# Optimization experiments

Hardware: AMD Instinct MI355X
Metric: run time of the kernel (lower is better)

## Reference

```python
import jax, jax.numpy as jnp
import numpy as np

SEQ, BS, IN, HS = 512, 64, 1024, 1024


def _xavier(key, shape):
    fan_in, fan_out = shape
    limit = np.sqrt(6.0 / (fan_in + fan_out)).astype(np.float32)
    return jax.random.uniform(key, shape, jnp.float32, -limit, limit)


def setup_inputs() -> dict:
    key = jax.random.key(0)
    k1, k2, k3, k4, k5 = jax.random.split(key, 5)
    return {
        "x": jax.random.normal(k1, (SEQ, BS, IN), jnp.float32),
        "h0": jax.random.normal(k2, (1, BS, HS), jnp.float32),
        "c0": jax.random.normal(k3, (1, BS, HS), jnp.float32),
        "weight_ih": _xavier(k4, (IN, 4 * HS)),
        "weight_hh": _xavier(k5, (HS, 4 * HS)),
        "bias": jnp.zeros((4 * HS,), jnp.float32),
    }


def reference(x, h0, c0, weight_ih, weight_hh, bias):
    HSd = weight_hh.shape[0]
    # Precompute the input projection for all timesteps in one big GEMM.
    x_gates = jnp.einsum('sbi,ih->sbh', x, weight_ih) + bias  # [S, B, 4H]

    def step(carry, xg_t):
        h_t, c_t = carry
        gates = xg_t + h_t @ weight_hh  # [B, 4H]
        i_t = jax.nn.sigmoid(gates[:, :HSd])
        f_t = jax.nn.sigmoid(gates[:, HSd:2 * HSd])
        g_t = jnp.tanh(gates[:, 2 * HSd:3 * HSd])
        o_t = jax.nn.sigmoid(gates[:, 3 * HSd:])
        c_t = f_t * c_t + i_t * g_t
        h_t = o_t * jnp.tanh(c_t)
        return (h_t, c_t), h_t

    (h_T, c_T), hidden_seq = jax.lax.scan(step, (h0[0], c0[0]), x_gates)
    return hidden_seq, (h_T[None], c_T[None])
```

## Files before the change

### kernel.cpp

```cpp
#include <hip/hip_runtime.h>
#include <stdint.h>


typedef unsigned short u16;
typedef __attribute__((ext_vector_type(8))) short bf16x8;
typedef __attribute__((ext_vector_type(2))) uint64_t u64x2;
typedef __attribute__((ext_vector_type(4))) float f32x4;

static __device__ __forceinline__ u16 f2b(float f) {
  uint32_t b = __float_as_uint(f);
  return (u16)((b + 0x7fffu + ((b >> 16) & 1u)) >> 16);
}
static __device__ __forceinline__ uint64_t pack4(float4 v) {
  return (uint64_t)f2b(v.x) | ((uint64_t)f2b(v.y) << 16) |
         ((uint64_t)f2b(v.z) << 32) | ((uint64_t)f2b(v.w) << 48);
}
static __device__ __forceinline__ float b2f(u16 u) {
  return __uint_as_float(((uint32_t)u) << 16);
}
static __device__ __forceinline__ float sigm(float x) {
  return 1.0f / (1.0f + __expf(-x));
}
static __device__ __forceinline__ float tanh_(float x) {
  float e = __expf(2.0f * x);
  return 1.0f - 2.0f / (e + 1.0f);
}

__global__ __launch_bounds__(256) void transpose_w(const float* __restrict__ Wih,
                                                   const float* __restrict__ Whh,
                                                   u16* __restrict__ Tih,
                                                   u16* __restrict__ Thh) {
  __shared__ float tile[64][65];
  const float* src = blockIdx.z ? Whh : Wih;
  u16* dst = blockIdx.z ? Thh : Tih;
  int k0 = blockIdx.y * 64, n0 = blockIdx.x * 64;
  int tid = threadIdx.x;
#pragma unroll
  for (int i = 0; i < 16; ++i) {
    int idx = i * 256 + tid;
    int kl = idx >> 6, nl = idx & 63;
    tile[kl][nl] = src[(size_t)(k0 + kl) * 4096 + n0 + nl];
  }
  __syncthreads();
#pragma unroll
  for (int i = 0; i < 16; ++i) {
    int idx = i * 256 + tid;
    int nl = idx >> 6, kl = idx & 63;
    dst[(size_t)(n0 + nl) * 1024 + k0 + kl] = f2b(tile[kl][nl]);
  }
}

__global__ __launch_bounds__(256) void convert_h0(const float* __restrict__ h0,
                                                  uint64_t* __restrict__ dst) {
  int i = blockIdx.x * 256 + threadIdx.x;
  float2 v = ((const float2*)h0)[i];
  uint32_t pair = (uint32_t)f2b(v.x) | ((uint32_t)f2b(v.y) << 16);
  dst[i] = (uint64_t)pair;
}

__global__ __launch_bounds__(256) void gemm_xg(const float* __restrict__ A,
                                               const u16* __restrict__ Bt,
                                               const float* __restrict__ bias,
                                               u16* __restrict__ C) {
  __shared__ u16 sA[2][128 * 32];
  __shared__ u16 sB[2][128 * 32];
  const int tid = threadIdx.x;
  const int wave = tid >> 6, lane = tid & 63;
  const int bx = blockIdx.x, by = blockIdx.y;
  const int wr = wave >> 1, wc = wave & 1;
  const int lm = lane & 15, ko = (lane >> 4) * 8;

  const int ar = lane >> 1, ac = (lane & 1) * 16;
  const float* gA = A + (size_t)(by * 128 + wave * 32 + ar) * 1024 + ac;
  const u16* gB = Bt + (size_t)(bx * 128 + wave * 32 + (lane >> 2)) * 1024 + (lane & 3) * 8;
  const int bidx = wave * 1024 + (lane >> 2) * 32 + (lane & 3) * 8;

  f32x4 acc[4][4] = {};

  auto stage = [&](int kt, int buf) {
    const u16* gb = gB + kt * 32;
    bf16x8 b0 = *(const bf16x8*)gb;
    bf16x8 b1 = *(const bf16x8*)(gb + 16 * 1024);
    *(bf16x8*)&sB[buf][bidx] = b0;
    *(bf16x8*)&sB[buf][bidx + 512] = b1;
    const float* ga = gA + kt * 32;
    float4 v0 = *(const float4*)(ga + 0);
    float4 v1 = *(const float4*)(ga + 4);
    float4 v2 = *(const float4*)(ga + 8);
    float4 v3 = *(const float4*)(ga + 12);
    uint64_t* la = (uint64_t*)&sA[buf][wave * 1024 + ar * 32 + ac];
    la[0] = pack4(v0);
    la[1] = pack4(v1);
    la[2] = pack4(v2);
    la[3] = pack4(v3);
  };

  stage(0, 0);
  __syncthreads();
  int p = 0;
  for (int kt = 0; kt < 32; ++kt) {
    if (kt < 31) stage(kt + 1, p ^ 1);
    bf16x8 af[4], bfv[4];
#pragma unroll
    for (int i = 0; i < 4; ++i)
      af[i] = *(const bf16x8*)&sA[p][(wr * 64 + i * 16 + lm) * 32 + ko];
#pragma unroll
    for (int j = 0; j < 4; ++j)
      bfv[j] = *(const bf16x8*)&sB[p][(wc * 64 + j * 16 + lm) * 32 + ko];
#pragma unroll
    for (int i = 0; i < 4; ++i)
#pragma unroll
      for (int j = 0; j < 4; ++j)
        acc[i][j] = __builtin_amdgcn_mfma_f32_16x16x32_bf16(af[i], bfv[j], acc[i][j], 0, 0, 0);
    __syncthreads();
    p ^= 1;
  }

  float bj[4];
#pragma unroll
  for (int j = 0; j < 4; ++j)
    bj[j] = bias[bx * 128 + wc * 64 + j * 16 + lm];
#pragma unroll
  for (int i = 0; i < 4; ++i) {
    int row = by * 128 + wr * 64 + i * 16 + (lane >> 4) * 4;
#pragma unroll
    for (int j = 0; j < 4; ++j) {
      int col = bx * 128 + wc * 64 + j * 16 + lm;
#pragma unroll
      for (int r = 0; r < 4; ++r)
        C[(size_t)(row + r) * 4096 + col] = f2b(acc[i][j][r] + bj[j]);
    }
  }
}

__global__ __launch_bounds__(512, 1) void recur_pers(
    const u16* __restrict__ xg,
    const u16* __restrict__ whh_t,
    uint64_t* __restrict__ h_tag,
    float* __restrict__ c_st,
    float* __restrict__ out_h,
    float* __restrict__ out_hT, float* __restrict__ out_cT,
    int t0, int W) {
  __shared__ float xchg[8][16][68];

  const int tid = threadIdx.x;
  const int wave = tid >> 6, lane = tid & 63;
  const int bid = blockIdx.x;
  const int un = bid & 63;
  const int bq = bid >> 6;
  const int lm = lane & 15, hi = lane >> 4;

  bf16x8 bfr[4][4];
#pragma unroll
  for (int nt = 0; nt < 4; ++nt) {
    const u16* bp = whh_t + (size_t)(nt * 1024 + un * 16 + lm) * 1024 + wave * 128 + hi * 8;
#pragma unroll
    for (int kk = 0; kk < 4; ++kk) bfr[kk][nt] = *(const bf16x8*)(bp + kk * 32);
  }

  const int r_b = tid >> 4, u = tid & 15;
  const int b = bq * 16 + r_b;
  const int unit = un * 16 + u;
  float c_val = (tid < 256) ? c_st[b * 1024 + unit] : 0.f;

  const int b_row = bq * 16 + lm;

  for (int ts = 0; ts < W; ++ts) {
    const int t = t0 + ts;

    u16 xr0 = 0, xr1 = 0, xr2 = 0, xr3 = 0;
    if (tid < 256) {
      const u16* xgp = xg + ((size_t)ts * 64 + b) * 4096 + unit;
      xr0 = xgp[0];
      xr1 = xgp[1024];
      xr2 = xgp[2048];
      xr3 = xgp[3072];
    }

    const uint64_t* hb = h_tag + ((size_t)((t - 1) & 1) * 64 + b_row) * 512 +
                         wave * 64 + hi * 4;
    uint64_t wbuf[16];
    {
      uint32_t spin = 0;
      bool ok = false;
      for (; spin < (1u << 15); ++spin) {
#pragma unroll
        for (int kk = 0; kk < 4; ++kk)
#pragma unroll
          for (int j = 0; j < 4; ++j)
            wbuf[kk * 4 + j] = __hip_atomic_load(hb + kk * 16 + j, __ATOMIC_RELAXED,
                                                 __HIP_MEMORY_SCOPE_AGENT);
        bool good = true;
#pragma unroll
        for (int i = 0; i < 16; ++i)
          good &= ((uint32_t)(wbuf[i] >> 32) >= (uint32_t)t);
        if (__all(good)) { ok = true; break; }
        __builtin_amdgcn_s_sleep(1);
      }
      if (!ok && lane == 0)
        out_h[(size_t)t * 65536 + bid] = 1.0e6f;
    }

    f32x4 acc[4] = {};
#pragma unroll
    for (int kk = 0; kk < 4; ++kk) {
      u64x2 v;
      v.x = (uint64_t)(uint32_t)wbuf[kk * 4 + 0] |
            ((uint64_t)(uint32_t)wbuf[kk * 4 + 1] << 32);
      v.y = (uint64_t)(uint32_t)wbuf[kk * 4 + 2] |
            ((uint64_t)(uint32_t)wbuf[kk * 4 + 3] << 32);
      bf16x8 a = __builtin_bit_cast(bf16x8, v);
#pragma unroll
      for (int nt = 0; nt < 4; ++nt)
        acc[nt] = __builtin_amdgcn_mfma_f32_16x16x32_bf16(a, bfr[kk][nt], acc[nt], 0, 0, 0);
    }
    {
      int crow = hi * 4;
#pragma unroll
      for (int nt = 0; nt < 4; ++nt)
#pragma unroll
        for (int r = 0; r < 4; ++r) xchg[wave][crow + r][nt * 16 + lm] = acc[nt][r];
    }
    __syncthreads();

    if (tid < 256) {
      float raw[4];
#pragma unroll
      for (int g = 0; g < 4; ++g) {
        int c = g * 16 + u;
        float s = xchg[0][r_b][c];
#pragma unroll
        for (int w = 1; w < 8; ++w) s += xchg[w][r_b][c];
        raw[g] = s;
      }
      float ig = sigm(raw[0] + b2f(xr0));
      float fg = sigm(raw[1] + b2f(xr1));
      float gg = tanh_(raw[2] + b2f(xr2));
      float og = sigm(raw[3] + b2f(xr3));
      c_val = fg * c_val + ig * gg;
      float h_new = og * tanh_(c_val);
      uint32_t mine = f2b(h_new);
      uint32_t other = __shfl_xor(mine, 1);
      if ((u & 1) == 0) {
        uint64_t word = (uint64_t)(mine | (other << 16)) | ((uint64_t)(uint32_t)(t + 1) << 32);
        __hip_atomic_store(
            h_tag + ((size_t)(t & 1) * 64 + b) * 512 + (unit >> 1), word,
            __ATOMIC_RELAXED, __HIP_MEMORY_SCOPE_AGENT);
      }
      out_h[(size_t)t * 65536 + (size_t)b * 1024 + unit] = h_new;
      if (t == 511) {
        out_hT[b * 1024 + unit] = h_new;
        out_cT[b * 1024 + unit] = c_val;
      }
    }
    __syncthreads();
  }

  if (tid < 256) c_st[b * 1024 + unit] = c_val;
}

extern "C" void kernel_launch(void* const* d_in, const int* in_sizes, int n_in,
                              void* d_out, int out_size, void* d_ws, size_t ws_size,
                              hipStream_t stream) {
  const float* x = (const float*)d_in[0];
  const float* h0 = (const float*)d_in[1];
  const float* c0 = (const float*)d_in[2];
  const float* wih = (const float*)d_in[3];
  const float* whh = (const float*)d_in[4];
  const float* bias = (const float*)d_in[5];

  float* out = (float*)d_out;
  float* out_h = out;
  float* out_hT = out + (size_t)512 * 64 * 1024;
  float* out_cT = out_hT + 64 * 1024;

  const size_t fixed = (size_t)2 * 4096 * 1024 * 2
                       + (size_t)2 * 64 * 512 * 8
                       + (size_t)64 * 1024 * 4;
  int W = 64;
  while (W > 4 && fixed + (size_t)W * 64 * 4096 * 2 > ws_size) W >>= 2;

  char* ws = (char*)d_ws;
  u16* wih_t = (u16*)ws;     ws += (size_t)4096 * 1024 * 2;
  u16* whh_t = (u16*)ws;     ws += (size_t)4096 * 1024 * 2;
  u16* xg = (u16*)ws;        ws += (size_t)W * 64 * 4096 * 2;
  uint64_t* h_tag = (uint64_t*)ws; ws += (size_t)2 * 64 * 512 * 8;
  float* c_st = (float*)ws;

  hipMemsetAsync(h_tag, 0, (size_t)2 * 64 * 512 * 8, stream);
  convert_h0<<<128, 256, 0, stream>>>(h0, h_tag + (size_t)64 * 512);
  hipMemcpyAsync(c_st, c0, (size_t)64 * 1024 * 4, hipMemcpyDeviceToDevice, stream);
  transpose_w<<<dim3(64, 16, 2), 256, 0, stream>>>(wih, whh, wih_t, whh_t);

  for (int t0 = 0; t0 < 512; t0 += W) {
    gemm_xg<<<dim3(32, W / 2), 256, 0, stream>>>(x + (size_t)t0 * 64 * 1024, wih_t, bias, xg);
    int t0c = t0, Wc = W;
    void* args[] = {(void*)&xg,    (void*)&whh_t,  (void*)&h_tag, (void*)&c_st,
                    (void*)&out_h, (void*)&out_hT, (void*)&out_cT,
                    (void*)&t0c,   (void*)&Wc};
    hipLaunchCooperativeKernel((const void*)recur_pers, dim3(256), dim3(512), args, 0,
                               stream);
  }
}
```

Measured before the change: 4.014 ms.

## Halve persistent grid and interleave two batch quarters per block

The persistent recurrent kernel now launches 128 blocks instead of 256. Each block keeps its slice of W_hh in registers and processes two batch quarters in alternating phases, with double-buffered LDS for the cross-wave reduction. This halves the number of blocks that must synchronise through the global h flags, and the wait for one batch group may overlap the compute of the other. In exchange each block does twice the serial work per timestep. The spin limit is also halved, and the sync between phases is removed, which relies on the alternating xchg buffers for LDS safety.

```diff
diff --git a/kernel.cpp b/kernel.cpp
--- a/kernel.cpp
+++ b/kernel.cpp
@@ -141,13 +141,13 @@
     float* __restrict__ out_h,
     float* __restrict__ out_hT, float* __restrict__ out_cT,
     int t0, int W) {
-  __shared__ float xchg[8][16][68];
+  __shared__ float xchg[2][8][16][68];
 
   const int tid = threadIdx.x;
   const int wave = tid >> 6, lane = tid & 63;
   const int bid = blockIdx.x;
-  const int un = bid & 63;
-  const int bq = bid >> 6;
+  const int un = bid >> 1;
+  const int p = bid & 1;
   const int lm = lane & 15, hi = lane >> 4;
 
   bf16x8 bfr[4][4];
@@ -159,31 +159,22 @@
   }
 
   const int r_b = tid >> 4, u = tid & 15;
-  const int b = bq * 16 + r_b;
   const int unit = un * 16 + u;
-  float c_val = (tid < 256) ? c_st[b * 1024 + unit] : 0.f;
-
-  const int b_row = bq * 16 + lm;
-
-  for (int ts = 0; ts < W; ++ts) {
-    const int t = t0 + ts;
-
-    u16 xr0 = 0, xr1 = 0, xr2 = 0, xr3 = 0;
-    if (tid < 256) {
-      const u16* xgp = xg + ((size_t)ts * 64 + b) * 4096 + unit;
-      xr0 = xgp[0];
-      xr1 = xgp[1024];
-      xr2 = xgp[2048];
-      xr3 = xgp[3072];
-    }
-
-    const uint64_t* hb = h_tag + ((size_t)((t - 1) & 1) * 64 + b_row) * 512 +
+  const int bqA = 2 * p, bqB = 2 * p + 1;
+  const int bA = bqA * 16 + r_b;
+  const int bB = bqB * 16 + r_b;
+  float cA = (tid < 256) ? c_st[bA * 1024 + unit] : 0.f;
+  float cB = (tid < 256) ? c_st[bB * 1024 + unit] : 0.f;
+
+  auto phase = [&](int s, int bq, int b, float& c_val, int t,
+                   u16 xr0, u16 xr1, u16 xr2, u16 xr3) {
+    const uint64_t* hb = h_tag + ((size_t)((t - 1) & 1) * 64 + bq * 16 + lm) * 512 +
                          wave * 64 + hi * 4;
     uint64_t wbuf[16];
     {
       uint32_t spin = 0;
       bool ok = false;
-      for (; spin < (1u << 15); ++spin) {
+      for (; spin < (1u << 14); ++spin) {
 #pragma unroll
         for (int kk = 0; kk < 4; ++kk)
 #pragma unroll
@@ -198,7 +189,7 @@
         __builtin_amdgcn_s_sleep(1);
       }
       if (!ok && lane == 0)
-        out_h[(size_t)t * 65536 + bid] = 1.0e6f;
+        out_h[(size_t)t * 65536 + bid * 2 + s] = 1.0e6f;
     }
 
     f32x4 acc[4] = {};
@@ -219,7 +210,7 @@
 #pragma unroll
       for (int nt = 0; nt < 4; ++nt)
 #pragma unroll
-        for (int r = 0; r < 4; ++r) xchg[wave][crow + r][nt * 16 + lm] = acc[nt][r];
+        for (int r = 0; r < 4; ++r) xchg[s][wave][crow + r][nt * 16 + lm] = acc[nt][r];
     }
     __syncthreads();
 
@@ -228,10 +219,10 @@
 #pragma unroll
       for (int g = 0; g < 4; ++g) {
         int c = g * 16 + u;
-        float s = xchg[0][r_b][c];
-#pragma unroll
-        for (int w = 1; w < 8; ++w) s += xchg[w][r_b][c];
-        raw[g] = s;
+        float sum = xchg[s][0][r_b][c];
+#pragma unroll
+        for (int w = 1; w < 8; ++w) sum += xchg[s][w][r_b][c];
+        raw[g] = sum;
       }
       float ig = sigm(raw[0] + b2f(xr0));
       float fg = sigm(raw[1] + b2f(xr1));
@@ -253,10 +244,25 @@
         out_cT[b * 1024 + unit] = c_val;
       }
     }
-    __syncthreads();
-  }
-
-  if (tid < 256) c_st[b * 1024 + unit] = c_val;
+  };
+
+  for (int ts = 0; ts < W; ++ts) {
+    const int t = t0 + ts;
+    u16 a0 = 0, a1 = 0, a2 = 0, a3 = 0, b0 = 0, b1 = 0, b2 = 0, b3 = 0;
+    if (tid < 256) {
+      const u16* xga = xg + ((size_t)ts * 64 + bA) * 4096 + unit;
+      const u16* xgb = xg + ((size_t)ts * 64 + bB) * 4096 + unit;
+      a0 = xga[0]; a1 = xga[1024]; a2 = xga[2048]; a3 = xga[3072];
+      b0 = xgb[0]; b1 = xgb[1024]; b2 = xgb[2048]; b3 = xgb[3072];
+    }
+    phase(0, bqA, bA, cA, t, a0, a1, a2, a3);
+    phase(1, bqB, bB, cB, t, b0, b1, b2, b3);
+  }
+
+  if (tid < 256) {
+    c_st[bA * 1024 + unit] = cA;
+    c_st[bB * 1024 + unit] = cB;
+  }
 }
 
 extern "C" void kernel_launch(void* const* d_in, const int* in_sizes, int n_in,
@@ -298,7 +304,7 @@
     void* args[] = {(void*)&xg,    (void*)&whh_t,  (void*)&h_tag, (void*)&c_st,
                     (void*)&out_h, (void*)&out_hT, (void*)&out_cT,
                     (void*)&t0c,   (void*)&Wc};
-    hipLaunchCooperativeKernel((const void*)recur_pers, dim3(256), dim3(512), args, 0,
+    hipLaunchCooperativeKernel((const void*)recur_pers, dim3(128), dim3(512), args, 0,
                                stream);
   }
 }
```

Result: slower. 5.088 ms (+26.8%).

## Halve recurrent block to 256 threads and stage W_hh slices in LDS

Applied to the files above, without the earlier changes.

The persistent LSTM recurrence kernel now runs 4 waves per block instead of 8, each wave covering twice the K range (8 MFMA k-steps). W_hh fragments move from registers into shared memory, and the cross-wave reduction drops from 8 partials to 4. This aims to cut per-step reduction and sync overhead and remove the idle half of threads in the gate phase. In exchange each wave must spin-load twice as many h words and read B fragments from LDS every step, which lengthens the serial critical path.

```diff
diff --git a/kernel.cpp b/kernel.cpp
--- a/kernel.cpp
+++ b/kernel.cpp
@@ -133,7 +133,7 @@
   }
 }
 
-__global__ __launch_bounds__(512, 1) void recur_pers(
+__global__ __launch_bounds__(256, 1) void recur_pers(
     const u16* __restrict__ xg,
     const u16* __restrict__ whh_t,
     uint64_t* __restrict__ h_tag,
@@ -141,7 +141,8 @@
     float* __restrict__ out_h,
     float* __restrict__ out_hT, float* __restrict__ out_cT,
     int t0, int W) {
-  __shared__ float xchg[8][16][68];
+  __shared__ u16 sW[4][8][4][512];
+  __shared__ float xchg[4][16][68];
 
   const int tid = threadIdx.x;
   const int wave = tid >> 6, lane = tid & 63;
@@ -150,49 +151,43 @@
   const int bq = bid >> 6;
   const int lm = lane & 15, hi = lane >> 4;
 
-  bf16x8 bfr[4][4];
-#pragma unroll
-  for (int nt = 0; nt < 4; ++nt) {
-    const u16* bp = whh_t + (size_t)(nt * 1024 + un * 16 + lm) * 1024 + wave * 128 + hi * 8;
-#pragma unroll
-    for (int kk = 0; kk < 4; ++kk) bfr[kk][nt] = *(const bf16x8*)(bp + kk * 32);
-  }
+#pragma unroll
+  for (int kk = 0; kk < 8; ++kk)
+#pragma unroll
+    for (int nt = 0; nt < 4; ++nt) {
+      const u16* bp = whh_t + (size_t)(nt * 1024 + un * 16 + lm) * 1024 +
+                      wave * 256 + kk * 32 + hi * 8;
+      *(bf16x8*)&sW[wave][kk][nt][lane * 8] = *(const bf16x8*)bp;
+    }
+  __syncthreads();
 
   const int r_b = tid >> 4, u = tid & 15;
   const int b = bq * 16 + r_b;
   const int unit = un * 16 + u;
-  float c_val = (tid < 256) ? c_st[b * 1024 + unit] : 0.f;
-
-  const int b_row = bq * 16 + lm;
+  float c_val = c_st[b * 1024 + unit];
 
   for (int ts = 0; ts < W; ++ts) {
     const int t = t0 + ts;
 
-    u16 xr0 = 0, xr1 = 0, xr2 = 0, xr3 = 0;
-    if (tid < 256) {
-      const u16* xgp = xg + ((size_t)ts * 64 + b) * 4096 + unit;
-      xr0 = xgp[0];
-      xr1 = xgp[1024];
-      xr2 = xgp[2048];
-      xr3 = xgp[3072];
-    }
-
-    const uint64_t* hb = h_tag + ((size_t)((t - 1) & 1) * 64 + b_row) * 512 +
-                         wave * 64 + hi * 4;
-    uint64_t wbuf[16];
+    const u16* xgp = xg + ((size_t)ts * 64 + b) * 4096 + unit;
+    u16 xr0 = xgp[0], xr1 = xgp[1024], xr2 = xgp[2048], xr3 = xgp[3072];
+
+    const uint64_t* hb = h_tag + ((size_t)((t - 1) & 1) * 64 + bq * 16 + lm) * 512 +
+                         wave * 128 + hi * 4;
+    uint64_t wbuf[32];
     {
       uint32_t spin = 0;
       bool ok = false;
       for (; spin < (1u << 15); ++spin) {
 #pragma unroll
-        for (int kk = 0; kk < 4; ++kk)
+        for (int kk = 0; kk < 8; ++kk)
 #pragma unroll
           for (int j = 0; j < 4; ++j)
             wbuf[kk * 4 + j] = __hip_atomic_load(hb + kk * 16 + j, __ATOMIC_RELAXED,
                                                  __HIP_MEMORY_SCOPE_AGENT);
         bool good = true;
 #pragma unroll
-        for (int i = 0; i < 16; ++i)
+        for (int i = 0; i < 32; ++i)
           good &= ((uint32_t)(wbuf[i] >> 32) >= (uint32_t)t);
         if (__all(good)) { ok = true; break; }
         __builtin_amdgcn_s_sleep(1);
@@ -203,7 +198,7 @@
 
     f32x4 acc[4] = {};
 #pragma unroll
-    for (int kk = 0; kk < 4; ++kk) {
+    for (int kk = 0; kk < 8; ++kk) {
       u64x2 v;
       v.x = (uint64_t)(uint32_t)wbuf[kk * 4 + 0] |
             ((uint64_t)(uint32_t)wbuf[kk * 4 + 1] << 32);
@@ -211,8 +206,10 @@
             ((uint64_t)(uint32_t)wbuf[kk * 4 + 3] << 32);
       bf16x8 a = __builtin_bit_cast(bf16x8, v);
 #pragma unroll
-      for (int nt = 0; nt < 4; ++nt)
-        acc[nt] = __builtin_amdgcn_mfma_f32_16x16x32_bf16(a, bfr[kk][nt], acc[nt], 0, 0, 0);
+      for (int nt = 0; nt < 4; ++nt) {
+        bf16x8 bf = *(const bf16x8*)&sW[wave][kk][nt][lane * 8];
+        acc[nt] = __builtin_amdgcn_mfma_f32_16x16x32_bf16(a, bf, acc[nt], 0, 0, 0);
+      }
     }
     {
       int crow = hi * 4;
@@ -223,15 +220,12 @@
     }
     __syncthreads();
 
-    if (tid < 256) {
+    {
       float raw[4];
 #pragma unroll
       for (int g = 0; g < 4; ++g) {
         int c = g * 16 + u;
-        float s = xchg[0][r_b][c];
-#pragma unroll
-        for (int w = 1; w < 8; ++w) s += xchg[w][r_b][c];
-        raw[g] = s;
+        raw[g] = xchg[0][r_b][c] + xchg[1][r_b][c] + xchg[2][r_b][c] + xchg[3][r_b][c];
       }
       float ig = sigm(raw[0] + b2f(xr0));
       float fg = sigm(raw[1] + b2f(xr1));
@@ -256,7 +250,7 @@
     __syncthreads();
   }
 
-  if (tid < 256) c_st[b * 1024 + unit] = c_val;
+  c_st[b * 1024 + unit] = c_val;
 }
 
 extern "C" void kernel_launch(void* const* d_in, const int* in_sizes, int n_in,
@@ -298,7 +292,7 @@
     void* args[] = {(void*)&xg,    (void*)&whh_t,  (void*)&h_tag, (void*)&c_st,
                     (void*)&out_h, (void*)&out_hT, (void*)&out_cT,
                     (void*)&t0c,   (void*)&Wc};
-    hipLaunchCooperativeKernel((const void*)recur_pers, dim3(256), dim3(512), args, 0,
+    hipLaunchCooperativeKernel((const void*)recur_pers, dim3(256), dim3(256), args, 0,
                                stream);
   }
 }
```

Measured after the change: 4.651 ms. 15.9% more time.
